# Kernel optimization log

Hardware: AMD Instinct MI355X
Metric: run time of the kernel (lower is better)

Reference implementation:

```python
import jax, jax.numpy as jnp
import numpy as np

N_NODES = 100000
N_EDGES = 3200000
N_FEAT = 128
N_GRAPHS = 64


def setup_inputs() -> dict:
    key = jax.random.key(0)
    ks = jax.random.split(key, 8)
    x = jax.random.normal(ks[0], (N_NODES, N_FEAT), dtype=jnp.float32)
    edge_index = jax.random.randint(ks[1], (2, N_EDGES), 0, N_NODES, dtype=jnp.int64)
    batch = jnp.sort(jax.random.randint(ks[2], (N_NODES,), 0, N_GRAPHS, dtype=jnp.int64))
    # GCNConv weights (glorot-style scale) and biases
    W1 = jax.random.normal(ks[3], (N_FEAT, 32), dtype=jnp.float32) / np.sqrt(N_FEAT)
    b1 = jnp.zeros((32,), dtype=jnp.float32)
    W2 = jax.random.normal(ks[4], (32, 16), dtype=jnp.float32) / np.sqrt(32.0)
    b2 = jnp.zeros((16,), dtype=jnp.float32)
    lin_w = jax.random.normal(ks[5], (16, 1), dtype=jnp.float32) / np.sqrt(16.0)
    lin_b = jnp.zeros((1,), dtype=jnp.float32)
    return {"x": x, "edge_index": edge_index, "batch": batch,
            "W1": W1, "b1": b1, "W2": W2, "b2": b2,
            "lin_w": lin_w, "lin_b": lin_b}


def _gcn_conv(x, W, b, src, dst, deg_inv_sqrt, n_nodes):
    # transform first (fewer features downstream when out_dim < in_dim)
    xw = x @ W  # [N, out]
    norm = deg_inv_sqrt[src] * deg_inv_sqrt[dst]  # [E+N]
    msg = xw[src] * norm[:, None]  # gather + scale
    out = jax.ops.segment_sum(msg, dst, num_segments=n_nodes)  # scatter-add
    return out + b


def reference(x, edge_index, batch, W1, b1, W2, b2, lin_w, lin_b):
    n_nodes = x.shape[0]
    self_loop = jnp.arange(n_nodes, dtype=edge_index.dtype)
    src = jnp.concatenate([edge_index[0], self_loop])
    dst = jnp.concatenate([edge_index[1], self_loop])
    # symmetric GCN normalization with self-loops
    deg = jax.ops.segment_sum(jnp.ones_like(src, dtype=x.dtype), dst,
                              num_segments=n_nodes)
    deg_inv_sqrt = jnp.where(deg > 0, jax.lax.rsqrt(jnp.maximum(deg, 1.0)), 0.0)

    h = _gcn_conv(x, W1, b1, src, dst, deg_inv_sqrt, n_nodes)
    h = jax.nn.relu(h)
    # F.dropout with training=False (eval) is identity
    h = _gcn_conv(h, W2, b2, src, dst, deg_inv_sqrt, n_nodes)

    # global_mean_pool over batch index
    sums = jax.ops.segment_sum(h, batch, num_segments=N_GRAPHS)  # [G,16]
    cnts = jax.ops.segment_sum(jnp.ones((n_nodes,), dtype=h.dtype), batch,
                               num_segments=N_GRAPHS)
    pooled = sums / jnp.maximum(cnts, 1.0)[:, None]
    return pooled @ lin_w + lin_b  # [G,1]
```

## Files before the change

### kernel.cpp

```cpp
#include <hip/hip_runtime.h>

#define NN 100000
#define NE 3200000
#define NF 128
#define C1 32
#define C2 16
#define NG 64
#define BKT_SH 7
#define BKT_W  128
#define NBKT   782
#define CH     8192
#define NW     391
#define RSTR   784
#define MAPCAP 6400

#define OFF_BCNT  0
#define OFF_BST   1024
#define OFF_RUN   2048
#define OFF_ROW   308608
#define OFF_DIS   408624
#define OFF_POOL  508624
#define OFF_CNTF  509648
#define OFF_EDG   509712
#define OFF_XS1H0 OFF_EDG
#define OFF_XS1H1 (OFF_EDG + NN*8)
#define OFF_H1A   (OFF_EDG + NE)
#define OFF_XS2B  (OFF_H1A + NN*16)
#define OFF_COL   (OFF_XS2B + NN*8)

__device__ __forceinline__ unsigned pack_bf2(float a, float b) {
    unsigned ua = __float_as_uint(a);
    unsigned ub = __float_as_uint(b);
    ua = (ua + 0x7fffu + ((ua >> 16) & 1u)) >> 16;
    ub = (ub + 0x7fffu + ((ub >> 16) & 1u)) & 0xffff0000u;
    return ua | ub;
}
__device__ __forceinline__ float2 unpack_bf2(unsigned u) {
    return make_float2(__uint_as_float(u << 16), __uint_as_float(u & 0xffff0000u));
}
__device__ __forceinline__ void acc4(float4& a, uint2 q) {
    float2 f0 = unpack_bf2(q.x), f1 = unpack_bf2(q.y);
    a.x += f0.x; a.y += f0.y; a.z += f1.x; a.w += f1.y;
}

__global__ __launch_bounds__(256) void k_part(
    const int* __restrict__ S, const int* __restrict__ D,
    unsigned* __restrict__ edgebuf, int* __restrict__ runstart,
    int* __restrict__ bcnt)
{
    __shared__ int lhist[1024];
    __shared__ int lstart[1024];
    __shared__ int lcur[NBKT];
    __shared__ int sd[256];
    __shared__ unsigned lsort[CH];
    const int w = blockIdx.x;
    const int t = threadIdx.x;
    const int e0 = w * CH;
    const int n = min(CH, NE - e0);

    for (int i = t; i < 1024; i += 256) lhist[i] = 0;
    __syncthreads();
    for (int i = t; i < n; i += 256)
        atomicAdd(&lhist[(unsigned)D[e0 + i] >> BKT_SH], 1);
    __syncthreads();
    for (int i = t; i < NBKT; i += 256) atomicAdd(&bcnt[i], lhist[i]);
    int c0 = lhist[t * 4 + 0], c1 = lhist[t * 4 + 1];
    int c2 = lhist[t * 4 + 2], c3 = lhist[t * 4 + 3];
    int ts = c0 + c1 + c2 + c3;
    sd[t] = ts;
    __syncthreads();
    for (int off = 1; off < 256; off <<= 1) {
        int v = (t >= off) ? sd[t - off] : 0;
        __syncthreads();
        sd[t] += v;
        __syncthreads();
    }
    int excl = sd[t] - ts;
    lstart[t * 4 + 0] = excl;
    lstart[t * 4 + 1] = excl + c0;
    lstart[t * 4 + 2] = excl + c0 + c1;
    lstart[t * 4 + 3] = excl + c0 + c1 + c2;
    __syncthreads();
    for (int i = t; i < 783; i += 256) runstart[w * RSTR + i] = lstart[i];
    for (int i = t; i < NBKT; i += 256) lcur[i] = lstart[i];
    __syncthreads();
    for (int i = t; i < n; i += 256) {
        int s = S[e0 + i], d = D[e0 + i];
        int pos = atomicAdd(&lcur[(unsigned)d >> BKT_SH], 1);
        lsort[pos] = ((unsigned)s << BKT_SH) | (unsigned)(d & (BKT_W - 1));
    }
    __syncthreads();
    for (int i = t; i < n; i += 256) edgebuf[e0 + i] = lsort[i];
}

__global__ __launch_bounds__(256) void k_bscan(const int* __restrict__ bcnt,
                                               int* __restrict__ bstart,
                                               int* __restrict__ rowstart) {
    __shared__ int sd[256];
    const int t = threadIdx.x;
    const int base = t * 4;
    int c0 = (base + 0 < NBKT) ? bcnt[base + 0] : 0;
    int c1 = (base + 1 < NBKT) ? bcnt[base + 1] : 0;
    int c2 = (base + 2 < NBKT) ? bcnt[base + 2] : 0;
    int c3 = (base + 3 < NBKT) ? bcnt[base + 3] : 0;
    int ts = c0 + c1 + c2 + c3;
    sd[t] = ts;
    __syncthreads();
    for (int off = 1; off < 256; off <<= 1) {
        int v = (t >= off) ? sd[t - off] : 0;
        __syncthreads();
        sd[t] += v;
        __syncthreads();
    }
    int excl = sd[t] - ts;
    if (base + 0 < 783) bstart[base + 0] = excl;
    if (base + 1 < 783) bstart[base + 1] = excl + c0;
    if (base + 2 < 783) bstart[base + 2] = excl + c0 + c1;
    if (base + 3 < 783) bstart[base + 3] = excl + c0 + c1 + c2;
    if (t == 0) rowstart[NN] = NE;
}

__global__ __launch_bounds__(256) void k_fillfused(
    const unsigned* __restrict__ edgebuf, const int* __restrict__ runstart,
    const int* __restrict__ bstart,
    int* __restrict__ rowstart, float* __restrict__ dis, int* __restrict__ colidx)
{
    __shared__ int rl[NW];
    __shared__ int pfx[NW];
    __shared__ int basea[NW];
    __shared__ unsigned short map[MAPCAP];
    __shared__ int lcnt[BKT_W];
    __shared__ int lcur[BKT_W];
    __shared__ int sd[256];
    const int b = blockIdx.x;
    const int t = threadIdx.x;
    const int bs = bstart[b];
    const int total = bstart[b + 1] - bs;

    for (int w = t; w < NW; w += 256) {
        int s0 = runstart[w * RSTR + b];
        int s1 = runstart[w * RSTR + b + 1];
        basea[w] = s0;
        rl[w] = s1 - s0;
    }
    if (t < BKT_W) lcnt[t] = 0;
    __syncthreads();
    {
        int w0 = t * 2;
        int c0 = (w0 < NW) ? rl[w0] : 0;
        int c1 = (w0 + 1 < NW) ? rl[w0 + 1] : 0;
        int ts = c0 + c1;
        sd[t] = ts;
        __syncthreads();
        for (int off = 1; off < 256; off <<= 1) {
            int v = (t >= off) ? sd[t - off] : 0;
            __syncthreads();
            sd[t] += v;
            __syncthreads();
        }
        int excl = sd[t] - ts;
        if (w0 < NW)     pfx[w0]     = excl;
        if (w0 + 1 < NW) pfx[w0 + 1] = excl + c0;
    }
    __syncthreads();
    for (int w = t; w < NW; w += 256) {
        int p = pfx[w], len = rl[w];
        basea[w] = w * CH + basea[w] - p;
        for (int i = 0; i < len; ++i) map[p + i] = (unsigned short)w;
    }
    __syncthreads();
    for (int j = t; j < total; j += 256) {
        unsigned p = edgebuf[basea[map[j]] + j];
        atomicAdd(&lcnt[p & (BKT_W - 1)], 1);
    }
    __syncthreads();
    if (t < BKT_W) lcur[t] = lcnt[t];
    __syncthreads();
    for (int off = 1; off < BKT_W; off <<= 1) {
        int v = (t < BKT_W && t >= off) ? lcur[t - off] : 0;
        __syncthreads();
        if (t < BKT_W) lcur[t] += v;
        __syncthreads();
    }
    if (t < BKT_W) {
        int excl = lcur[t] - lcnt[t];
        int node = b * BKT_W + t;
        if (node < NN) {
            rowstart[node] = bs + excl;
            dis[node] = rsqrtf((float)lcnt[t] + 1.0f);
        }
        lcur[t] = bs + excl;
    }
    __syncthreads();
    for (int j = t; j < total; j += 256) {
        unsigned p = edgebuf[basea[map[j]] + j];
        int pos = atomicAdd(&lcur[p & (BKT_W - 1)], 1);
        colidx[pos] = (int)(p >> BKT_SH);
    }
}

__global__ __launch_bounds__(256) void k_gemm1(
    const float* __restrict__ x, const float* __restrict__ W1,
    const float* __restrict__ dis,
    unsigned* __restrict__ xs1h0, unsigned* __restrict__ xs1h1)
{
    __shared__ float xls[128 * 33];
    __shared__ float wls[32 * 32];
    const int t = threadIdx.x;
    const int tc = t & 7;
    const int tr = t >> 3;
    const int base = blockIdx.x * 128;

    float a[4][4] = {};

    for (int k0 = 0; k0 < NF; k0 += 32) {
        {
            int i = t * 4;
            int kk = i >> 5, c = i & 31;
            *(float4*)&wls[kk * 32 + c] = *(const float4*)&W1[(k0 + kk) * C1 + c];
        }
        #pragma unroll
        for (int r = 0; r < 4; ++r) {
            int n = (t >> 3) + r * 32;
            int j = (t & 7) * 4;
            int node = base + n;
            float4 v = make_float4(0.f, 0.f, 0.f, 0.f);
            if (node < NN) v = *(const float4*)&x[(long long)node * NF + k0 + j];
            xls[n * 33 + j + 0] = v.x;
            xls[n * 33 + j + 1] = v.y;
            xls[n * 33 + j + 2] = v.z;
            xls[n * 33 + j + 3] = v.w;
        }
        __syncthreads();
        #pragma unroll 8
        for (int kk = 0; kk < 32; ++kk) {
            float4 w = *(const float4*)&wls[kk * 32 + tc * 4];
            #pragma unroll
            for (int i = 0; i < 4; ++i) {
                float xv = xls[(tr * 4 + i) * 33 + kk];
                a[i][0] = fmaf(xv, w.x, a[i][0]);
                a[i][1] = fmaf(xv, w.y, a[i][1]);
                a[i][2] = fmaf(xv, w.z, a[i][2]);
                a[i][3] = fmaf(xv, w.w, a[i][3]);
            }
        }
        __syncthreads();
    }
    #pragma unroll
    for (int i = 0; i < 4; ++i) {
        int node = base + tr * 4 + i;
        if (node < NN) {
            float dv = dis[node];
            uint2 o;
            o.x = pack_bf2(a[i][0] * dv, a[i][1] * dv);
            o.y = pack_bf2(a[i][2] * dv, a[i][3] * dv);
            unsigned* dst = (tc < 4) ? &xs1h0[node * 8 + tc * 2]
                                     : &xs1h1[node * 8 + (tc - 4) * 2];
            *(uint2*)dst = o;
        }
    }
}

template<int HALF>
__global__ __launch_bounds__(256) void k_gather1h(
    const unsigned* __restrict__ xsh, const int* __restrict__ colidx,
    const int* __restrict__ rowstart, const float* __restrict__ dis,
    const float* __restrict__ b1, float* __restrict__ h1a,
    const float* __restrict__ W2, unsigned* __restrict__ xs2b)
{
    __shared__ float w2s[C1 * C2];
    __shared__ float hrow[64 * 33];
    const int t = threadIdx.x;
    if (HALF == 1 && t < 128) *(float4*)&w2s[t * 4] = *(const float4*)&W2[t * 4];
    const int l = t & 3;
    const int n = t >> 2;
    const int v = blockIdx.x * 64 + n;
    const bool valid = v < NN;

    float4 acc = make_float4(0.f, 0.f, 0.f, 0.f);
    float dv = 0.f;
    if (valid) {
        const int start = rowstart[v];
        const int num = rowstart[v + 1] - start;
        const int* __restrict__ cp = &colidx[start];
        uint2 u = *(const uint2*)&xsh[v * 8 + l * 2];
        float4 a0 = make_float4(0.f, 0.f, 0.f, 0.f);
        acc4(a0, u);
        float4 a1 = make_float4(0.f, 0.f, 0.f, 0.f), a2 = a1, a3 = a1;
        int i = 0;
        for (; i + 8 <= num; i += 8) {
            int s0 = cp[i], s1 = cp[i+1], s2 = cp[i+2], s3 = cp[i+3];
            int s4 = cp[i+4], s5 = cp[i+5], s6 = cp[i+6], s7 = cp[i+7];
            uint2 q0 = *(const uint2*)&xsh[s0 * 8 + l * 2];
            uint2 q1 = *(const uint2*)&xsh[s1 * 8 + l * 2];
            uint2 q2 = *(const uint2*)&xsh[s2 * 8 + l * 2];
            uint2 q3 = *(const uint2*)&xsh[s3 * 8 + l * 2];
            uint2 q4 = *(const uint2*)&xsh[s4 * 8 + l * 2];
            uint2 q5 = *(const uint2*)&xsh[s5 * 8 + l * 2];
            uint2 q6 = *(const uint2*)&xsh[s6 * 8 + l * 2];
            uint2 q7 = *(const uint2*)&xsh[s7 * 8 + l * 2];
            acc4(a0, q0); acc4(a1, q1); acc4(a2, q2); acc4(a3, q3);
            acc4(a0, q4); acc4(a1, q5); acc4(a2, q6); acc4(a3, q7);
        }
        for (; i < num; ++i) {
            uint2 q = *(const uint2*)&xsh[cp[i] * 8 + l * 2];
            acc4(a0, q);
        }
        acc.x = (a0.x + a1.x) + (a2.x + a3.x);
        acc.y = (a0.y + a1.y) + (a2.y + a3.y);
        acc.z = (a0.z + a1.z) + (a2.z + a3.z);
        acc.w = (a0.w + a1.w) + (a2.w + a3.w);
        dv = dis[v];
    }

    if (HALF == 0) {
        if (valid) {
            float4 o;
            o.x = fmaxf(fmaf(acc.x, dv, b1[l * 4 + 0]), 0.f);
            o.y = fmaxf(fmaf(acc.y, dv, b1[l * 4 + 1]), 0.f);
            o.z = fmaxf(fmaf(acc.z, dv, b1[l * 4 + 2]), 0.f);
            o.w = fmaxf(fmaf(acc.w, dv, b1[l * 4 + 3]), 0.f);
            *(float4*)&h1a[v * 16 + l * 4] = o;
        }
    } else {
        if (valid) {
            float4 hh = *(const float4*)&h1a[v * 16 + l * 4];
            hrow[n * 33 + l * 4 + 0] = hh.x;
            hrow[n * 33 + l * 4 + 1] = hh.y;
            hrow[n * 33 + l * 4 + 2] = hh.z;
            hrow[n * 33 + l * 4 + 3] = hh.w;
            hrow[n * 33 + 16 + l * 4 + 0] = fmaxf(fmaf(acc.x, dv, b1[16 + l * 4 + 0]), 0.f);
            hrow[n * 33 + 16 + l * 4 + 1] = fmaxf(fmaf(acc.y, dv, b1[16 + l * 4 + 1]), 0.f);
            hrow[n * 33 + 16 + l * 4 + 2] = fmaxf(fmaf(acc.z, dv, b1[16 + l * 4 + 2]), 0.f);
            hrow[n * 33 + 16 + l * 4 + 3] = fmaxf(fmaf(acc.w, dv, b1[16 + l * 4 + 3]), 0.f);
        }
        __syncthreads();
        if (valid) {
            const float* hr = &hrow[n * 33];
            float s0 = 0.f, s1 = 0.f, s2 = 0.f, s3 = 0.f;
            #pragma unroll
            for (int k = 0; k < 32; ++k) {
                float hv = hr[k];
                s0 = fmaf(hv, w2s[k * C2 + l * 4 + 0], s0);
                s1 = fmaf(hv, w2s[k * C2 + l * 4 + 1], s1);
                s2 = fmaf(hv, w2s[k * C2 + l * 4 + 2], s2);
                s3 = fmaf(hv, w2s[k * C2 + l * 4 + 3], s3);
            }
            uint2 o;
            o.x = pack_bf2(s0 * dv, s1 * dv);
            o.y = pack_bf2(s2 * dv, s3 * dv);
            *(uint2*)&xs2b[v * 8 + l * 2] = o;
        }
    }
}

__global__ __launch_bounds__(256) void k_gather2(
    const unsigned* __restrict__ xs2b, const int* __restrict__ colidx,
    const int* __restrict__ rowstart, const float* __restrict__ dis,
    const int* __restrict__ batch,
    float* __restrict__ pool, float* __restrict__ cntf)
{
    __shared__ float psum[NG * C2];
    __shared__ float cs[NG];
    const int t = threadIdx.x;
    for (int i = t; i < NG * C2; i += 256) psum[i] = 0.f;
    if (t < NG) cs[t] = 0.f;
    __syncthreads();

    const int l = t & 3;
    const int n = t >> 2;
    const int v = blockIdx.x * 64 + n;
    if (v < NN) {
        const int start = rowstart[v];
        const int num = rowstart[v + 1] - start;
        const int* __restrict__ cp = &colidx[start];
        uint2 u = *(const uint2*)&xs2b[v * 8 + l * 2];
        float4 a0 = make_float4(0.f, 0.f, 0.f, 0.f);
        acc4(a0, u);
        float4 a1 = make_float4(0.f, 0.f, 0.f, 0.f), a2 = a1, a3 = a1;
        int i = 0;
        for (; i + 8 <= num; i += 8) {
            int s0 = cp[i], s1 = cp[i+1], s2 = cp[i+2], s3 = cp[i+3];
            int s4 = cp[i+4], s5 = cp[i+5], s6 = cp[i+6], s7 = cp[i+7];
            uint2 q0 = *(const uint2*)&xs2b[s0 * 8 + l * 2];
            uint2 q1 = *(const uint2*)&xs2b[s1 * 8 + l * 2];
            uint2 q2 = *(const uint2*)&xs2b[s2 * 8 + l * 2];
            uint2 q3 = *(const uint2*)&xs2b[s3 * 8 + l * 2];
            uint2 q4 = *(const uint2*)&xs2b[s4 * 8 + l * 2];
            uint2 q5 = *(const uint2*)&xs2b[s5 * 8 + l * 2];
            uint2 q6 = *(const uint2*)&xs2b[s6 * 8 + l * 2];
            uint2 q7 = *(const uint2*)&xs2b[s7 * 8 + l * 2];
            acc4(a0, q0); acc4(a1, q1); acc4(a2, q2); acc4(a3, q3);
            acc4(a0, q4); acc4(a1, q5); acc4(a2, q6); acc4(a3, q7);
        }
        for (; i < num; ++i) {
            uint2 q = *(const uint2*)&xs2b[cp[i] * 8 + l * 2];
            acc4(a0, q);
        }
        float ax = (a0.x + a1.x) + (a2.x + a3.x);
        float ay = (a0.y + a1.y) + (a2.y + a3.y);
        float az = (a0.z + a1.z) + (a2.z + a3.z);
        float aw = (a0.w + a1.w) + (a2.w + a3.w);
        float dv = dis[v];
        int g = batch[v];
        atomicAdd(&psum[g * C2 + l * 4 + 0], ax * dv);
        atomicAdd(&psum[g * C2 + l * 4 + 1], ay * dv);
        atomicAdd(&psum[g * C2 + l * 4 + 2], az * dv);
        atomicAdd(&psum[g * C2 + l * 4 + 3], aw * dv);
        if (l == 0) atomicAdd(&cs[g], 1.0f);
    }
    __syncthreads();
    for (int i = t; i < NG * C2; i += 256)
        if (psum[i] != 0.f) atomicAdd(&pool[i], psum[i]);
    if (t < NG && cs[t] != 0.f) atomicAdd(&cntf[t], cs[t]);
}

__global__ void k_final(const float* __restrict__ pool, const float* __restrict__ cntf,
                        const float* __restrict__ b2,
                        const float* __restrict__ lw, const float* __restrict__ lb,
                        float* __restrict__ out)
{
    int g = threadIdx.x;
    if (g < NG) {
        float c = fmaxf(cntf[g], 1.0f);
        float inv = 1.0f / c;
        float s = lb[0];
        #pragma unroll
        for (int k = 0; k < C2; ++k) {
            s = fmaf(b2[k], lw[k], s);
            s = fmaf(pool[g * C2 + k] * inv, lw[k], s);
        }
        out[g] = s;
    }
}

extern "C" void kernel_launch(void* const* d_in, const int* in_sizes, int n_in,
                              void* d_out, int out_size, void* d_ws, size_t ws_size,
                              hipStream_t stream) {
    const float* x     = (const float*)d_in[0];
    const int*   ei    = (const int*)d_in[1];
    const int*   batch = (const int*)d_in[2];
    const float* W1    = (const float*)d_in[3];
    const float* b1    = (const float*)d_in[4];
    const float* W2    = (const float*)d_in[5];
    const float* b2    = (const float*)d_in[6];
    const float* lw    = (const float*)d_in[7];
    const float* lb    = (const float*)d_in[8];
    float* out = (float*)d_out;

    float*    wsf = (float*)d_ws;
    int*      wsi = (int*)d_ws;
    unsigned* wsu = (unsigned*)d_ws;

    int*      bcnt     = wsi + OFF_BCNT;
    int*      bstart   = wsi + OFF_BST;
    int*      runstart = wsi + OFF_RUN;
    int*      rowstart = wsi + OFF_ROW;
    float*    dis      = wsf + OFF_DIS;
    float*    pool     = wsf + OFF_POOL;
    float*    cntf     = wsf + OFF_CNTF;
    unsigned* edgebuf  = wsu + OFF_EDG;
    unsigned* xs1h0    = wsu + OFF_XS1H0;
    unsigned* xs1h1    = wsu + OFF_XS1H1;
    float*    h1a      = wsf + OFF_H1A;
    unsigned* xs2b     = wsu + OFF_XS2B;
    int*      colidx   = wsi + OFF_COL;

    const int* S = ei;
    const int* D = ei + NE;

    hipMemsetAsync(bcnt, 0, 1024 * sizeof(int), stream);
    hipMemsetAsync(pool, 0, (NG * C2 + NG) * sizeof(float), stream);

    k_part       <<<NW, 256, 0, stream>>>(S, D, edgebuf, runstart, bcnt);
    k_bscan      <<<1, 256, 0, stream>>>(bcnt, bstart, rowstart);
    k_fillfused  <<<NBKT, 256, 0, stream>>>(edgebuf, runstart, bstart, rowstart, dis, colidx);
    k_gemm1      <<<(NN + 127) / 128, 256, 0, stream>>>(x, W1, dis, xs1h0, xs1h1);
    k_gather1h<0><<<(NN + 63) / 64, 256, 0, stream>>>(xs1h0, colidx, rowstart, dis, b1, h1a, W2, xs2b);
    k_gather1h<1><<<(NN + 63) / 64, 256, 0, stream>>>(xs1h1, colidx, rowstart, dis, b1, h1a, W2, xs2b);
    k_gather2    <<<(NN + 63) / 64, 256, 0, stream>>>(xs2b, colidx, rowstart, dis, batch, pool, cntf);
    k_final      <<<1, 64, 0, stream>>>(pool, cntf, b2, lw, lb, out);
}
```

Measured before the change: 280.2 us.

## Fuse two half-feature layer-1 gathers into one kernel and halve partition chunk size

Merges the two k_gather1h passes, which each gathered half of the 32 layer-1 features, into a single k_gather1 kernel. It uses 8 lanes per node so both halves are gathered at once, which removes the h1a intermediate round trip and one launch. Each node's colidx list is now read once instead of twice. Separately, the partition chunk size drops from 8192 to 4096 edges, doubling the k_part block count to 782 and widening the per-thread prefix scan in the fill kernel to 4 runs. This adds more runs per bucket to merge, and each gather block now covers only 32 nodes.

```diff
diff --git a/kernel.cpp b/kernel.cpp
--- a/kernel.cpp
+++ b/kernel.cpp
@@ -9,23 +9,22 @@
 #define BKT_SH 7
 #define BKT_W  128
 #define NBKT   782
-#define CH     8192
-#define NW     391
+#define CH     4096
+#define NW     782
 #define RSTR   784
 #define MAPCAP 6400
 
 #define OFF_BCNT  0
 #define OFF_BST   1024
 #define OFF_RUN   2048
-#define OFF_ROW   308608
-#define OFF_DIS   408624
-#define OFF_POOL  508624
-#define OFF_CNTF  509648
-#define OFF_EDG   509712
+#define OFF_ROW   615136
+#define OFF_DIS   715140
+#define OFF_POOL  815140
+#define OFF_CNTF  816164
+#define OFF_EDG   816240
 #define OFF_XS1H0 OFF_EDG
 #define OFF_XS1H1 (OFF_EDG + NN*8)
-#define OFF_H1A   (OFF_EDG + NE)
-#define OFF_XS2B  (OFF_H1A + NN*16)
+#define OFF_XS2B  (OFF_EDG + NE)
 #define OFF_COL   (OFF_XS2B + NN*8)
 
 __device__ __forceinline__ unsigned pack_bf2(float a, float b) {
@@ -146,10 +145,12 @@
     if (t < BKT_W) lcnt[t] = 0;
     __syncthreads();
     {
-        int w0 = t * 2;
-        int c0 = (w0 < NW) ? rl[w0] : 0;
+        int w0 = t * 4;
+        int c0 = (w0 + 0 < NW) ? rl[w0 + 0] : 0;
         int c1 = (w0 + 1 < NW) ? rl[w0 + 1] : 0;
-        int ts = c0 + c1;
+        int c2 = (w0 + 2 < NW) ? rl[w0 + 2] : 0;
+        int c3 = (w0 + 3 < NW) ? rl[w0 + 3] : 0;
+        int ts = c0 + c1 + c2 + c3;
         sd[t] = ts;
         __syncthreads();
         for (int off = 1; off < 256; off <<= 1) {
@@ -159,8 +160,10 @@
             __syncthreads();
         }
         int excl = sd[t] - ts;
-        if (w0 < NW)     pfx[w0]     = excl;
+        if (w0 + 0 < NW) pfx[w0 + 0] = excl;
         if (w0 + 1 < NW) pfx[w0 + 1] = excl + c0;
+        if (w0 + 2 < NW) pfx[w0 + 2] = excl + c0 + c1;
+        if (w0 + 3 < NW) pfx[w0 + 3] = excl + c0 + c1 + c2;
     }
     __syncthreads();
     for (int w = t; w < NW; w += 256) {
@@ -261,29 +264,29 @@
     }
 }
 
-template<int HALF>
-__global__ __launch_bounds__(256) void k_gather1h(
-    const unsigned* __restrict__ xsh, const int* __restrict__ colidx,
-    const int* __restrict__ rowstart, const float* __restrict__ dis,
-    const float* __restrict__ b1, float* __restrict__ h1a,
+__global__ __launch_bounds__(256) void k_gather1(
+    const unsigned* __restrict__ xs1h0, const unsigned* __restrict__ xs1h1,
+    const int* __restrict__ colidx, const int* __restrict__ rowstart,
+    const float* __restrict__ dis, const float* __restrict__ b1,
     const float* __restrict__ W2, unsigned* __restrict__ xs2b)
 {
     __shared__ float w2s[C1 * C2];
-    __shared__ float hrow[64 * 33];
-    const int t = threadIdx.x;
-    if (HALF == 1 && t < 128) *(float4*)&w2s[t * 4] = *(const float4*)&W2[t * 4];
-    const int l = t & 3;
-    const int n = t >> 2;
-    const int v = blockIdx.x * 64 + n;
+    __shared__ float hrow[32 * 33];
+    const int t = threadIdx.x;
+    if (t < 128) *(float4*)&w2s[t * 4] = *(const float4*)&W2[t * 4];
+    const int l = t & 7;
+    const int lc = l & 3;
+    const int n = t >> 3;
+    const int v = blockIdx.x * 32 + n;
     const bool valid = v < NN;
-
-    float4 acc = make_float4(0.f, 0.f, 0.f, 0.f);
+    const unsigned* __restrict__ xsh = (l < 4) ? xs1h0 : xs1h1;
+
     float dv = 0.f;
     if (valid) {
         const int start = rowstart[v];
         const int num = rowstart[v + 1] - start;
         const int* __restrict__ cp = &colidx[start];
-        uint2 u = *(const uint2*)&xsh[v * 8 + l * 2];
+        uint2 u = *(const uint2*)&xsh[v * 8 + lc * 2];
         float4 a0 = make_float4(0.f, 0.f, 0.f, 0.f);
         acc4(a0, u);
         float4 a1 = make_float4(0.f, 0.f, 0.f, 0.f), a2 = a1, a3 = a1;
@@ -291,66 +294,43 @@
         for (; i + 8 <= num; i += 8) {
             int s0 = cp[i], s1 = cp[i+1], s2 = cp[i+2], s3 = cp[i+3];
             int s4 = cp[i+4], s5 = cp[i+5], s6 = cp[i+6], s7 = cp[i+7];
-            uint2 q0 = *(const uint2*)&xsh[s0 * 8 + l * 2];
-            uint2 q1 = *(const uint2*)&xsh[s1 * 8 + l * 2];
-            uint2 q2 = *(const uint2*)&xsh[s2 * 8 + l * 2];
-            uint2 q3 = *(const uint2*)&xsh[s3 * 8 + l * 2];
-            uint2 q4 = *(const uint2*)&xsh[s4 * 8 + l * 2];
-            uint2 q5 = *(const uint2*)&xsh[s5 * 8 + l * 2];
-            uint2 q6 = *(const uint2*)&xsh[s6 * 8 + l * 2];
-            uint2 q7 = *(const uint2*)&xsh[s7 * 8 + l * 2];
+            uint2 q0 = *(const uint2*)&xsh[s0 * 8 + lc * 2];
+            uint2 q1 = *(const uint2*)&xsh[s1 * 8 + lc * 2];
+            uint2 q2 = *(const uint2*)&xsh[s2 * 8 + lc * 2];
+            uint2 q3 = *(const uint2*)&xsh[s3 * 8 + lc * 2];
+            uint2 q4 = *(const uint2*)&xsh[s4 * 8 + lc * 2];
+            uint2 q5 = *(const uint2*)&xsh[s5 * 8 + lc * 2];
+            uint2 q6 = *(const uint2*)&xsh[s6 * 8 + lc * 2];
+            uint2 q7 = *(const uint2*)&xsh[s7 * 8 + lc * 2];
             acc4(a0, q0); acc4(a1, q1); acc4(a2, q2); acc4(a3, q3);
             acc4(a0, q4); acc4(a1, q5); acc4(a2, q6); acc4(a3, q7);
         }
         for (; i < num; ++i) {
-            uint2 q = *(const uint2*)&xsh[cp[i] * 8 + l * 2];
+            uint2 q = *(const uint2*)&xsh[cp[i] * 8 + lc * 2];
             acc4(a0, q);
         }
-        acc.x = (a0.x + a1.x) + (a2.x + a3.x);
-        acc.y = (a0.y + a1.y) + (a2.y + a3.y);
-        acc.z = (a0.z + a1.z) + (a2.z + a3.z);
-        acc.w = (a0.w + a1.w) + (a2.w + a3.w);
+        float ax = (a0.x + a1.x) + (a2.x + a3.x);
+        float ay = (a0.y + a1.y) + (a2.y + a3.y);
+        float az = (a0.z + a1.z) + (a2.z + a3.z);
+        float aw = (a0.w + a1.w) + (a2.w + a3.w);
         dv = dis[v];
-    }
-
-    if (HALF == 0) {
-        if (valid) {
-            float4 o;
-            o.x = fmaxf(fmaf(acc.x, dv, b1[l * 4 + 0]), 0.f);
-            o.y = fmaxf(fmaf(acc.y, dv, b1[l * 4 + 1]), 0.f);
-            o.z = fmaxf(fmaf(acc.z, dv, b1[l * 4 + 2]), 0.f);
-            o.w = fmaxf(fmaf(acc.w, dv, b1[l * 4 + 3]), 0.f);
-            *(float4*)&h1a[v * 16 + l * 4] = o;
-        }
-    } else {
-        if (valid) {
-            float4 hh = *(const float4*)&h1a[v * 16 + l * 4];
-            hrow[n * 33 + l * 4 + 0] = hh.x;
-            hrow[n * 33 + l * 4 + 1] = hh.y;
-            hrow[n * 33 + l * 4 + 2] = hh.z;
-            hrow[n * 33 + l * 4 + 3] = hh.w;
-            hrow[n * 33 + 16 + l * 4 + 0] = fmaxf(fmaf(acc.x, dv, b1[16 + l * 4 + 0]), 0.f);
-            hrow[n * 33 + 16 + l * 4 + 1] = fmaxf(fmaf(acc.y, dv, b1[16 + l * 4 + 1]), 0.f);
-            hrow[n * 33 + 16 + l * 4 + 2] = fmaxf(fmaf(acc.z, dv, b1[16 + l * 4 + 2]), 0.f);
-            hrow[n * 33 + 16 + l * 4 + 3] = fmaxf(fmaf(acc.w, dv, b1[16 + l * 4 + 3]), 0.f);
-        }
-        __syncthreads();
-        if (valid) {
-            const float* hr = &hrow[n * 33];
-            float s0 = 0.f, s1 = 0.f, s2 = 0.f, s3 = 0.f;
-            #pragma unroll
-            for (int k = 0; k < 32; ++k) {
-                float hv = hr[k];
-                s0 = fmaf(hv, w2s[k * C2 + l * 4 + 0], s0);
-                s1 = fmaf(hv, w2s[k * C2 + l * 4 + 1], s1);
-                s2 = fmaf(hv, w2s[k * C2 + l * 4 + 2], s2);
-                s3 = fmaf(hv, w2s[k * C2 + l * 4 + 3], s3);
-            }
-            uint2 o;
-            o.x = pack_bf2(s0 * dv, s1 * dv);
-            o.y = pack_bf2(s2 * dv, s3 * dv);
-            *(uint2*)&xs2b[v * 8 + l * 2] = o;
-        }
+        const int cb = (l < 4 ? 0 : 16) + lc * 4;
+        hrow[n * 33 + cb + 0] = fmaxf(fmaf(ax, dv, b1[cb + 0]), 0.f);
+        hrow[n * 33 + cb + 1] = fmaxf(fmaf(ay, dv, b1[cb + 1]), 0.f);
+        hrow[n * 33 + cb + 2] = fmaxf(fmaf(az, dv, b1[cb + 2]), 0.f);
+        hrow[n * 33 + cb + 3] = fmaxf(fmaf(aw, dv, b1[cb + 3]), 0.f);
+    }
+    __syncthreads();
+    if (valid) {
+        const float* hr = &hrow[n * 33];
+        float s0 = 0.f, s1 = 0.f;
+        #pragma unroll
+        for (int k = 0; k < 32; ++k) {
+            float hv = hr[k];
+            s0 = fmaf(hv, w2s[k * C2 + l * 2 + 0], s0);
+            s1 = fmaf(hv, w2s[k * C2 + l * 2 + 1], s1);
+        }
+        xs2b[v * 8 + l] = pack_bf2(s0 * dv, s1 * dv);
     }
 }
 
@@ -462,7 +442,6 @@
     unsigned* edgebuf  = wsu + OFF_EDG;
     unsigned* xs1h0    = wsu + OFF_XS1H0;
     unsigned* xs1h1    = wsu + OFF_XS1H1;
-    float*    h1a      = wsf + OFF_H1A;
     unsigned* xs2b     = wsu + OFF_XS2B;
     int*      colidx   = wsi + OFF_COL;
 
@@ -472,12 +451,11 @@
     hipMemsetAsync(bcnt, 0, 1024 * sizeof(int), stream);
     hipMemsetAsync(pool, 0, (NG * C2 + NG) * sizeof(float), stream);
 
-    k_part       <<<NW, 256, 0, stream>>>(S, D, edgebuf, runstart, bcnt);
-    k_bscan      <<<1, 256, 0, stream>>>(bcnt, bstart, rowstart);
-    k_fillfused  <<<NBKT, 256, 0, stream>>>(edgebuf, runstart, bstart, rowstart, dis, colidx);
-    k_gemm1      <<<(NN + 127) / 128, 256, 0, stream>>>(x, W1, dis, xs1h0, xs1h1);
-    k_gather1h<0><<<(NN + 63) / 64, 256, 0, stream>>>(xs1h0, colidx, rowstart, dis, b1, h1a, W2, xs2b);
-    k_gather1h<1><<<(NN + 63) / 64, 256, 0, stream>>>(xs1h1, colidx, rowstart, dis, b1, h1a, W2, xs2b);
-    k_gather2    <<<(NN + 63) / 64, 256, 0, stream>>>(xs2b, colidx, rowstart, dis, batch, pool, cntf);
-    k_final      <<<1, 64, 0, stream>>>(pool, cntf, b2, lw, lb, out);
-}
+    k_part     <<<NW, 256, 0, stream>>>(S, D, edgebuf, runstart, bcnt);
+    k_bscan    <<<1, 256, 0, stream>>>(bcnt, bstart, rowstart);
+    k_fillfused<<<NBKT, 256, 0, stream>>>(edgebuf, runstart, bstart, rowstart, dis, colidx);
+    k_gemm1    <<<(NN + 127) / 128, 256, 0, stream>>>(x, W1, dis, xs1h0, xs1h1);
+    k_gather1  <<<(NN + 31) / 32, 256, 0, stream>>>(xs1h0, xs1h1, colidx, rowstart, dis, b1, W2, xs2b);
+    k_gather2  <<<(NN + 63) / 64, 256, 0, stream>>>(xs2b, colidx, rowstart, dis, batch, pool, cntf);
+    k_final    <<<1, 64, 0, stream>>>(pool, cntf, b2, lw, lb, out);
+}
```

After: 302.8 us. +8.0%, slower.
